# Optimization experiments

Measured on AMD Instinct MI355X. Metric: run time of the kernel, lower is better.

## Reference

```python
import jax, jax.numpy as jnp
import numpy as np

KMEANS_ITERS = 3   # soft-kmeans refinement iterations
TOPK = 12          # hardcoded in the torch module
EPS = 1e-8


def _gather(x, idx):
    # batched_index_select: x (b, c, m); idx (b, n, k) -> (b, c, n, k)
    return jax.vmap(lambda xb, ib: xb[:, ib])(x, idx)


def _soft_kmeans(points, cent):
    # points (b, n, c); cent (b, m, c) -> refined centroids and soft assignment weights (b, n, m)
    for _ in range(KMEANS_ITERS):
        p2 = jnp.sum(points * points, axis=-1)           # (b, n)
        c2 = jnp.sum(cent * cent, axis=-1)               # (b, m)
        logits = -(p2[:, :, None] - 2.0 * jnp.einsum('bnc,bmc->bnm', points, cent) + c2[:, None, :])
        w = jax.nn.softmax(logits, axis=-1)              # (b, n, m)
        cent = jnp.einsum('bnm,bnc->bmc', w, points) / (jnp.sum(w, axis=1)[:, :, None] + EPS)
    return cent, w


def setup_inputs():
    key = jax.random.key(0)
    k1, k2, k3 = jax.random.split(key, 3)
    b, c, H, W, k = 4, 192, 80, 80, 9
    n = H * W
    out_c = 192
    x = jax.random.normal(k1, (b, c, n, 1), dtype=jnp.float32)
    edge_index = jax.random.randint(k2, (2, b, n, k), 0, n)
    conv_w = jax.random.normal(k3, (out_c, 3 * c), dtype=jnp.float32) * (1.0 / np.sqrt(3 * c))
    conv_b = jnp.zeros((out_c,), dtype=jnp.float32)
    return {"x": x, "edge_index": edge_index, "conv_w": conv_w, "conv_b": conv_b,
            "num_centroids": 50, "H": 80, "W": 80}


def reference(x, edge_index, conv_w, conv_b, num_centroids, H, W):
    b, c, n, _ = x.shape
    xs = x[..., 0]                                        # (b, c, n)
    # initial centroids: adaptive_avg_pool2d to (5, 10); H, W chosen divisible so bins are uniform
    x_img = xs.reshape(b, c, H, W)
    init_cent = x_img.reshape(b, c, 5, H // 5, 10, W // 10).mean(axis=(3, 5)).reshape(b, c, 50)
    # edge gathers + max-relative reduction
    x_i = _gather(xs, edge_index[1])                      # (b, c, n, k)
    x_j = _gather(xs, edge_index[0])                      # (b, c, n, k)
    x_j = jnp.max(x_j - x_i, axis=-1, keepdims=True)      # (b, c, n, 1)
    # soft-kmeans centroid construction
    points = jnp.transpose(xs, (0, 2, 1))                 # (b, n, c)
    cent, weights = _soft_kmeans(points, jnp.transpose(init_cent, (0, 2, 1)))
    cent = jnp.transpose(cent, (0, 2, 1))                 # (b, c, m)
    # topk centroid routing + second gather-max stage
    _, nn_idx = jax.lax.top_k(weights, TOPK)              # (b, n, 12)
    x_jc = _gather(cent, nn_idx)                          # (b, c, n, 12)
    x_jc = jnp.max(x_jc - xs[..., None], axis=-1, keepdims=True)  # (b, c, n, 1)
    # channel-interleaved concat (matches torch stack on dim=2 then reshape to 3c)
    feat = jnp.stack([x, x_j, x_jc], axis=2).reshape(b, 3 * c, n)  # (b, 3c, n)
    # BasicConv: 1x1 conv + bias + relu (norm=None)
    out = jnp.einsum('oi,bin->bon', conv_w, feat) + conv_b[None, :, None]
    return jax.nn.relu(out)[..., None]                    # (b, out_c, n, 1)
```

## Files before the change

### kernel.cpp

```cpp
#include <hip/hip_runtime.h>
#include <hip/hip_bf16.h>
#include <math.h>

#define B_   4
#define C_   192
#define N_   6400
#define K_   9
#define M_   50
#define TK_  12
#define OC_  192
#define KC_  576
#define CH_  100
#define LSTR 53
#define TSTR 72
#define XSTR 40
#define GSTR 40
#define FSTR 392

typedef __bf16 b16x8 __attribute__((ext_vector_type(8)));
typedef float f32x4 __attribute__((ext_vector_type(4)));

__device__ inline unsigned short f2b(float f) {
    union { __hip_bfloat16 h; unsigned short u; } v;
    v.h = __float2bfloat16(f);
    return v.u;
}
__device__ inline float b2f(unsigned short u) {
    union { float f; unsigned int i; } v;
    v.i = ((unsigned int)u) << 16;
    return v.f;
}
__device__ inline void up8(uint4 v, float* f) {
    unsigned int w[4] = {v.x, v.y, v.z, v.w};
#pragma unroll
    for (int i = 0; i < 4; i++) {
        f[2 * i]     = b2f((unsigned short)(w[i] & 0xffffu));
        f[2 * i + 1] = b2f((unsigned short)(w[i] >> 16));
    }
}
__device__ inline uint4 pack8(const float* f) {
    unsigned int w[4];
#pragma unroll
    for (int i = 0; i < 4; i++)
        w[i] = (unsigned int)f2b(f[2 * i]) | ((unsigned int)f2b(f[2 * i + 1]) << 16);
    uint4 v; v.x = w[0]; v.y = w[1]; v.z = w[2]; v.w = w[3];
    return v;
}

__global__ void k_transpose(const float* __restrict__ x, float* __restrict__ xt,
                            unsigned short* __restrict__ xt16,
                            unsigned short* __restrict__ xt16l,
                            const float* __restrict__ cw,
                            unsigned short* __restrict__ Wg16) {
    int tid = threadIdx.y * 32 + threadIdx.x;
    if (blockIdx.x >= 200) {
        int g = ((blockIdx.x - 200) * 24 + blockIdx.z * 6 + blockIdx.y) * 256 + tid;
        if (g < OC_ * KC_) {
            int r = g % KC_;
            Wg16[g] = f2b(cw[(g / KC_) * KC_ + (r % C_) * 3 + (r / C_)]);
        }
        return;
    }
    __shared__ float tile[32][33];
    int b = blockIdx.z;
    int p0 = blockIdx.x * 32, c0 = blockIdx.y * 32;
    int tx = threadIdx.x, ty = threadIdx.y;
    const float* xb = x + (size_t)b * C_ * N_;
    float* xtb = xt + (size_t)b * N_ * C_;
    unsigned short* xt16b = xt16 + (size_t)b * N_ * C_;
    unsigned short* xt16lb = xt16l + (size_t)b * N_ * C_;
#pragma unroll
    for (int i = 0; i < 4; i++) {
        int cc = ty + 8 * i;
        tile[cc][tx] = xb[(size_t)(c0 + cc) * N_ + p0 + tx];
    }
    __syncthreads();
#pragma unroll
    for (int i = 0; i < 4; i++) {
        int pp = ty + 8 * i;
        float v = tile[tx][pp];
        size_t o = (size_t)(p0 + pp) * C_ + c0 + tx;
        xtb[o] = v;
        unsigned short hi = f2b(v);
        xt16b[o] = hi;
        xt16lb[o] = f2b(v - b2f(hi));
    }
}

__global__ __launch_bounds__(192) void k_init_cent(const float* __restrict__ xt,
        float* __restrict__ cent, float* __restrict__ c2,
        unsigned short* __restrict__ centh, unsigned short* __restrict__ centl) {
    int m = blockIdx.x, b = blockIdx.y, c = threadIdx.x;
    if (m >= M_) {
        size_t o = ((size_t)b * 64 + m) * C_ + c;
        centh[o] = 0; centl[o] = 0;
        return;
    }
    int gy = m / 10, gx = m % 10;
    const float* xtb = xt + (size_t)b * N_ * C_;
    float s = 0.f;
    for (int yy = 0; yy < 16; yy++)
        for (int xx = 0; xx < 8; xx++) {
            int p = (gy * 16 + yy) * 80 + gx * 8 + xx;
            s += xtb[(size_t)p * C_ + c];
        }
    float v = s * (1.f / 128.f);
    cent[((size_t)b * M_ + m) * C_ + c] = v;
    size_t oh = ((size_t)b * 64 + m) * C_ + c;
    unsigned short hi = f2b(v);
    centh[oh] = hi;
    centl[oh] = f2b(v - b2f(hi));
    float q = v * v;
    __shared__ float red[3];
#pragma unroll
    for (int off = 32; off > 0; off >>= 1) q += __shfl_down(q, off, 64);
    if ((c & 63) == 0) red[c >> 6] = q;
    __syncthreads();
    if (c == 0) c2[(size_t)b * M_ + m] = red[0] + red[1] + red[2];
}

__global__ __launch_bounds__(512) void k_logits_upd(const float* __restrict__ xt,
        const unsigned short* __restrict__ xt16, const unsigned short* __restrict__ xt16l,
        const float* __restrict__ cent,
        const unsigned short* __restrict__ centh, const unsigned short* __restrict__ centl,
        const float* __restrict__ c2g,
        unsigned short* __restrict__ part, float* __restrict__ wsp,
        int* __restrict__ nn, int do_topk, int fast) {
    __shared__ alignas(16) char smem[51712];
    __shared__ float sred[512];
    float* lg = (float*)(smem + 20480);
    unsigned short* lgTh = (unsigned short*)smem;
    unsigned short* lgTl = (unsigned short*)(smem + 9216);
    unsigned short* xTh = (unsigned short*)(smem + 18432);
    unsigned short* xTl = (unsigned short*)(smem + 35072);
    int b = blockIdx.y;
    int blk = blockIdx.x;
    int p0 = blk * 64;
    int tid = threadIdx.x;
    int wave = tid >> 6, lane = tid & 63;
    int m16 = lane & 15, q = lane >> 4;
    const float* xb = xt + ((size_t)b * N_ + p0) * C_;
    const unsigned short* x16b = xt16 + ((size_t)b * N_ + p0) * C_;
    const unsigned short* x16lb = xt16l + ((size_t)b * N_ + p0) * C_;
    if (fast) {
        const unsigned short* chg = centh + (size_t)b * 64 * C_;
        const unsigned short* clg = centl + (size_t)b * 64 * C_;
        int pg = wave & 3, mh = wave >> 2;
        f32x4 acc1[2];
#pragma unroll
        for (int i = 0; i < 2; i++) acc1[i] = (f32x4){0.f, 0.f, 0.f, 0.f};
#pragma unroll
        for (int kt = 0; kt < 6; kt++) {
            int kg = kt * 32;
            size_t xo = (size_t)(pg * 16 + m16) * C_ + kg + q * 8;
            b16x8 bh = *(const b16x8*)&x16b[xo];
            b16x8 bl = *(const b16x8*)&x16lb[xo];
#pragma unroll
            for (int t = 0; t < 2; t++) {
                int mt = mh * 2 + t;
                size_t co = (size_t)(mt * 16 + m16) * C_ + kg + q * 8;
                b16x8 ah = *(const b16x8*)&chg[co];
                b16x8 al = *(const b16x8*)&clg[co];
                acc1[t] = __builtin_amdgcn_mfma_f32_16x16x32_bf16(ah, bh, acc1[t], 0, 0, 0);
                acc1[t] = __builtin_amdgcn_mfma_f32_16x16x32_bf16(ah, bl, acc1[t], 0, 0, 0);
                acc1[t] = __builtin_amdgcn_mfma_f32_16x16x32_bf16(al, bh, acc1[t], 0, 0, 0);
            }
        }
#pragma unroll
        for (int t = 0; t < 2; t++) {
#pragma unroll
            for (int r = 0; r < 4; r++) {
                int m = (mh * 2 + t) * 16 + q * 4 + r;
                if (m < M_) {
                    float c2v = c2g[(size_t)b * M_ + m];
                    lg[(pg * 16 + m16) * LSTR + m] = 2.f * acc1[t][r] - c2v;
                }
            }
        }
    } else {
        const float* cb = cent + (size_t)b * M_ * C_;
        int grp = tid >> 8;
        int ltid = tid & 255;
        int ltx = ltid & 15, lty = ltid >> 4;
        int llr = ltid >> 2, llq = ltid & 3;
        float* Acg = (float*)(smem + grp * 8704);
        float* Bpg = (float*)(smem + grp * 8704 + 4352);
        float acc[4][4];
#pragma unroll
        for (int i = 0; i < 4; i++)
#pragma unroll
            for (int j = 0; j < 4; j++) acc[i][j] = 0.f;
        for (int kt = 0; kt < 6; kt++) {
            int kg = (grp * 6 + kt) * 16;
            float4 cv = make_float4(0.f, 0.f, 0.f, 0.f);
            if (llr < M_) cv = *(const float4*)&cb[(size_t)llr * C_ + kg + 4 * llq];
            float4 pv = *(const float4*)&xb[(size_t)llr * C_ + kg + 4 * llq];
            __syncthreads();
            Acg[(4 * llq + 0) * 68 + llr] = cv.x; Acg[(4 * llq + 1) * 68 + llr] = cv.y;
            Acg[(4 * llq + 2) * 68 + llr] = cv.z; Acg[(4 * llq + 3) * 68 + llr] = cv.w;
            Bpg[(4 * llq + 0) * 68 + llr] = pv.x; Bpg[(4 * llq + 1) * 68 + llr] = pv.y;
            Bpg[(4 * llq + 2) * 68 + llr] = pv.z; Bpg[(4 * llq + 3) * 68 + llr] = pv.w;
            __syncthreads();
#pragma unroll
            for (int kk = 0; kk < 16; kk++) {
                float4 a = *(const float4*)&Acg[kk * 68 + 4 * lty];
                float4 bb = *(const float4*)&Bpg[kk * 68 + 4 * ltx];
                acc[0][0] += a.x * bb.x; acc[0][1] += a.x * bb.y; acc[0][2] += a.x * bb.z; acc[0][3] += a.x * bb.w;
                acc[1][0] += a.y * bb.x; acc[1][1] += a.y * bb.y; acc[1][2] += a.y * bb.z; acc[1][3] += a.y * bb.w;
                acc[2][0] += a.z * bb.x; acc[2][1] += a.z * bb.y; acc[2][2] += a.z * bb.z; acc[2][3] += a.z * bb.w;
                acc[3][0] += a.w * bb.x; acc[3][1] += a.w * bb.y; acc[3][2] += a.w * bb.z; acc[3][3] += a.w * bb.w;
            }
        }
        float* scr = (float*)(smem + 35072);
        if (grp == 1) {
#pragma unroll
            for (int i = 0; i < 4; i++)
#pragma unroll
                for (int j = 0; j < 4; j++) scr[ltid * 16 + i * 4 + j] = acc[i][j];
        }
        __syncthreads();
        if (grp == 0) {
#pragma unroll
            for (int i = 0; i < 4; i++) {
                int m = 4 * lty + i;
                if (m < M_) {
                    float c2v = c2g[(size_t)b * M_ + m];
#pragma unroll
                    for (int j = 0; j < 4; j++) {
                        float t = acc[i][j] + scr[ltid * 16 + i * 4 + j];
                        lg[(4 * ltx + j) * LSTR + m] = 2.f * t - c2v;
                    }
                }
            }
        }
    }
    __syncthreads();
    {
        int p = tid & 63, prt = tid >> 6;
        int m0 = prt * 7;
        int m1 = (m0 + 7 > M_) ? M_ : m0 + 7;
        float* row = &lg[p * LSTR];
        float mx = -1e30f;
        for (int m = m0; m < m1; m++) mx = fmaxf(mx, row[m]);
        sred[prt * 64 + p] = mx;
        __syncthreads();
        mx = -1e30f;
#pragma unroll
        for (int k = 0; k < 8; k++) mx = fmaxf(mx, sred[k * 64 + p]);
        float s = 0.f;
        for (int m = m0; m < m1; m++) {
            float e = expf(row[m] - mx);
            row[m] = e;
            s += e;
        }
        __syncthreads();
        sred[prt * 64 + p] = s;
        __syncthreads();
        s = 0.f;
#pragma unroll
        for (int k = 0; k < 8; k++) s += sred[k * 64 + p];
        float inv = 1.f / s;
        for (int m = m0; m < m1; m++) row[m] *= inv;
    }
    __syncthreads();
    for (int j = tid; j < 64 * 64; j += 512) {
        int m = j >> 6, p = j & 63;
        float w = (m < M_) ? lg[p * LSTR + m] : 0.f;
        unsigned short hi = f2b(w);
        lgTh[m * TSTR + p] = hi;
        lgTl[m * TSTR + p] = f2b(w - b2f(hi));
    }
    __syncthreads();
    if (do_topk && tid < 64) {
        float* row = &lg[tid * LSTR];
        int* nb = nn + ((size_t)b * N_ + p0 + tid) * TK_;
        for (int r = 0; r < TK_; r++) {
            float bv = -1.f;
            int bi = 0;
            for (int m = 0; m < M_; m++) {
                float v = row[m];
                if (v > bv) { bv = v; bi = m; }
            }
            nb[r] = bi;
            row[bi] = -1.f;
        }
    }
    int mt2 = wave >> 1, cbase = (wave & 1) * 7;
    f32x4 acc2[7];
#pragma unroll
    for (int i = 0; i < 7; i++) acc2[i] = (f32x4){0.f, 0.f, 0.f, 0.f};
    for (int h = 0; h < 2; h++) {
        __syncthreads();
        for (int j = tid; j < 32 * 24; j += 512) {
            int pl = j & 31, ko = (j >> 5) * 8;
            int4 vh = *(const int4*)&x16b[(size_t)(h * 32 + pl) * C_ + ko];
            int4 vl = *(const int4*)&x16lb[(size_t)(h * 32 + pl) * C_ + ko];
            const unsigned short* ph = (const unsigned short*)&vh;
            const unsigned short* pv = (const unsigned short*)&vl;
#pragma unroll
            for (int i = 0; i < 8; i++) {
                xTh[(ko + i) * XSTR + pl] = ph[i];
                xTl[(ko + i) * XSTR + pl] = pv[i];
            }
        }
        for (int j = tid; j < 32 * 16; j += 512) {
            int pl = j & 31, c = C_ + (j >> 5);
            xTh[c * XSTR + pl] = (c == C_) ? f2b(1.f) : 0;
            xTl[c * XSTR + pl] = 0;
        }
        __syncthreads();
        b16x8 ah = *(const b16x8*)&lgTh[(mt2 * 16 + m16) * TSTR + h * 32 + q * 8];
        b16x8 al = *(const b16x8*)&lgTl[(mt2 * 16 + m16) * TSTR + h * 32 + q * 8];
#pragma unroll
        for (int ci = 0; ci < 7; ci++) {
            int ct = cbase + ci;
            if (ct >= 13) continue;
            b16x8 bh = *(const b16x8*)&xTh[(ct * 16 + m16) * XSTR + q * 8];
            b16x8 bl = *(const b16x8*)&xTl[(ct * 16 + m16) * XSTR + q * 8];
            acc2[ci] = __builtin_amdgcn_mfma_f32_16x16x32_bf16(ah, bh, acc2[ci], 0, 0, 0);
            acc2[ci] = __builtin_amdgcn_mfma_f32_16x16x32_bf16(ah, bl, acc2[ci], 0, 0, 0);
            acc2[ci] = __builtin_amdgcn_mfma_f32_16x16x32_bf16(al, bh, acc2[ci], 0, 0, 0);
        }
    }
    unsigned short* pb = part + ((size_t)b * CH_ + blk) * (size_t)(M_ * C_);
    int mbase = mt2 * 16 + q * 4;
#pragma unroll
    for (int ci = 0; ci < 7; ci++) {
        int ct = cbase + ci;
        if (ct >= 13) continue;
        int c = ct * 16 + m16;
#pragma unroll
        for (int r = 0; r < 4; r++) {
            int mm = mbase + r;
            if (mm >= M_) continue;
            float v = acc2[ci][r];
            if (c < C_) pb[(size_t)mm * C_ + c] = f2b(v);
            else if (c == C_) wsp[((size_t)b * CH_ + blk) * M_ + mm] = v;
        }
    }
}

__global__ __launch_bounds__(768) void k_upd_reduce(const unsigned short* __restrict__ part,
        const float* __restrict__ wsp, float* __restrict__ cent, float* __restrict__ c2,
        unsigned short* __restrict__ cent16,
        unsigned short* __restrict__ centh, unsigned short* __restrict__ centl, int last) {
    int m = blockIdx.x, b = blockIdx.y;
    int tid = threadIdx.x;
    int c = tid % 192, g = tid / 192;
    __shared__ float pred[3][192];
    __shared__ float sws;
    __shared__ float red[3];
    const unsigned short* pp = part + (((size_t)b * CH_ + (size_t)g * 25) * M_ + m) * (size_t)C_ + c;
    float s = 0.f;
    for (int ch = 0; ch < 25; ch++)
        s += b2f(pp[(size_t)ch * M_ * C_]);
    if (g) pred[g - 1][c] = s;
    if (tid < 64) {
        float w = wsp[((size_t)b * CH_ + tid) * M_ + m];
        if (tid + 64 < CH_) w += wsp[((size_t)b * CH_ + tid + 64) * M_ + m];
#pragma unroll
        for (int off = 32; off > 0; off >>= 1) w += __shfl_down(w, off, 64);
        if (tid == 0) sws = w + 1e-8f;
    }
    __syncthreads();
    if (g == 0) {
        float v = (s + pred[0][c] + pred[1][c] + pred[2][c]) / sws;
        size_t o = ((size_t)b * M_ + m) * C_ + c;
        cent[o] = v;
        if (last) cent16[o] = f2b(v);
        size_t oh = ((size_t)b * 64 + m) * C_ + c;
        unsigned short hi = f2b(v);
        centh[oh] = hi;
        centl[oh] = f2b(v - b2f(hi));
        float q = v * v;
#pragma unroll
        for (int off = 32; off > 0; off >>= 1) q += __shfl_down(q, off, 64);
        if ((c & 63) == 0) red[c >> 6] = q;
    }
    __syncthreads();
    if (tid == 0) c2[(size_t)b * M_ + m] = red[0] + red[1] + red[2];
}

__global__ __launch_bounds__(256) void k_gemm(const unsigned short* __restrict__ Wg16,
        const unsigned short* __restrict__ xt16, const unsigned short* __restrict__ cent16,
        const int* __restrict__ edge, const int* __restrict__ nn,
        const float* __restrict__ bias, float* __restrict__ out) {
    __shared__ alignas(16) char smem[65536];
    unsigned short* feat = (unsigned short*)smem;
    int* sidx = (int*)(smem + 50176);
    short* As = (short*)(smem + 50176);
    int bid = blockIdx.x;
    int xcd = bid & 7;
    int b = xcd >> 1;
    int po = ((xcd & 1) * 50 + (bid >> 3)) * 64;
    int tid = threadIdx.x;
    int wave = tid >> 6, lane = tid & 63;
    int m16 = lane & 15, q = lane >> 4;
    const unsigned short* xb = xt16 + (size_t)b * N_ * C_;
    const unsigned short* cb = cent16 + (size_t)b * M_ * C_;
    for (int j = tid; j < 64 * 30; j += 256) {
        int g = j / 30, r = j % 30;
        size_t base = (size_t)b * N_ + po + g;
        int v;
        if (r < K_) v = edge[base * K_ + r];
        else if (r < 2 * K_) v = edge[(size_t)B_ * N_ * K_ + base * K_ + (r - K_)];
        else v = nn[base * TK_ + (r - 2 * K_)];
        sidx[j] = v;
    }
    __syncthreads();
#pragma unroll
    for (int r6 = 0; r6 < 6; r6++) {
        int j = r6 * 256 + tid;
        int g = j / 24, t = j % 24;
        int ch0 = t * 8;
        const int* si = &sidx[g * 30];
        int p = po + g;
        float xv[8], ta[8], tb[8], mj[8], mc[8];
        up8(*(const uint4*)&xb[(size_t)p * C_ + ch0], xv);
#pragma unroll
        for (int e = 0; e < 8; e++) { mj[e] = -1e30f; mc[e] = -1e30f; }
#pragma unroll
        for (int kk = 0; kk < K_; kk++) {
            up8(*(const uint4*)&xb[(size_t)si[kk] * C_ + ch0], ta);
            up8(*(const uint4*)&xb[(size_t)si[K_ + kk] * C_ + ch0], tb);
#pragma unroll
            for (int e = 0; e < 8; e++) mj[e] = fmaxf(mj[e], ta[e] - tb[e]);
        }
#pragma unroll
        for (int kk = 0; kk < TK_; kk++) {
            up8(*(const uint4*)&cb[(size_t)si[2 * K_ + kk] * C_ + ch0], ta);
#pragma unroll
            for (int e = 0; e < 8; e++) mc[e] = fmaxf(mc[e], ta[e]);
        }
#pragma unroll
        for (int e = 0; e < 8; e++) mc[e] -= xv[e];
        *(uint4*)&feat[(size_t)g * FSTR + ch0] = pack8(mj);
        *(uint4*)&feat[(size_t)g * FSTR + 192 + ch0] = pack8(mc);
    }
    f32x4 acc[12];
#pragma unroll
    for (int i = 0; i < 12; i++) acc[i] = (f32x4){0.f, 0.f, 0.f, 0.f};
    for (int kt = 0; kt < 18; kt++) {
        int kg = kt * 32;
        int4 av[3];
#pragma unroll
        for (int t = 0; t < 3; t++) {
            int idx = t * 256 + tid;
            av[t] = *(const int4*)&Wg16[(size_t)(idx >> 2) * KC_ + kg + (idx & 3) * 8];
        }
        __syncthreads();
#pragma unroll
        for (int t = 0; t < 3; t++) {
            int idx = t * 256 + tid;
            *(int4*)&As[(idx >> 2) * GSTR + (idx & 3) * 8] = av[t];
        }
        __syncthreads();
        b16x8 bf;
        if (kt < 6)
            bf = *(const b16x8*)&xb[(size_t)(po + wave * 16 + m16) * C_ + kg + q * 8];
        else
            bf = *(const b16x8*)&feat[(size_t)(wave * 16 + m16) * FSTR + (kg - C_) + q * 8];
#pragma unroll
        for (int of = 0; of < 12; of++) {
            b16x8 af = *(const b16x8*)&As[(of * 16 + m16) * GSTR + q * 8];
            acc[of] = __builtin_amdgcn_mfma_f32_16x16x32_bf16(af, bf, acc[of], 0, 0, 0);
        }
    }
    int p = po + wave * 16 + m16;
#pragma unroll
    for (int of = 0; of < 12; of++) {
        int o = of * 16 + q * 4;
        float4 bv = *(const float4*)&bias[o];
        float bia[4] = {bv.x, bv.y, bv.z, bv.w};
#pragma unroll
        for (int r = 0; r < 4; r++)
            out[((size_t)b * OC_ + o + r) * N_ + p] = fmaxf(acc[of][r] + bia[r], 0.f);
    }
}

extern "C" void kernel_launch(void* const* d_in, const int* in_sizes, int n_in,
                              void* d_out, int out_size, void* d_ws, size_t ws_size,
                              hipStream_t stream) {
    (void)in_sizes; (void)n_in; (void)out_size; (void)ws_size;
    const float* x   = (const float*)d_in[0];
    const int* edge  = (const int*)d_in[1];
    const float* cw  = (const float*)d_in[2];
    const float* cbi = (const float*)d_in[3];
    float* ws = (float*)d_ws;
    size_t o = 0;
    float* xt   = ws + o; o += (size_t)B_ * N_ * C_;
    unsigned short* xt16 = (unsigned short*)(ws + o); o += (size_t)B_ * N_ * C_ / 2;
    unsigned short* xt16l = (unsigned short*)(ws + o); o += (size_t)B_ * N_ * C_ / 2;
    unsigned short* Wg16 = (unsigned short*)(ws + o); o += (size_t)OC_ * KC_ / 2;
    float* cent = ws + o; o += (size_t)B_ * M_ * C_;
    unsigned short* cent16 = (unsigned short*)(ws + o); o += (size_t)B_ * M_ * C_ / 2;
    unsigned short* centh = (unsigned short*)(ws + o); o += (size_t)B_ * 64 * C_ / 2;
    unsigned short* centl = (unsigned short*)(ws + o); o += (size_t)B_ * 64 * C_ / 2;
    float* c2   = ws + o; o += (size_t)B_ * M_;
    unsigned short* part = (unsigned short*)(ws + o); o += (size_t)B_ * CH_ * M_ * C_ / 2;
    float* wsp  = ws + o; o += (size_t)B_ * CH_ * M_;
    int* nn = (int*)(ws + o); o += (size_t)B_ * N_ * TK_;
    float* outp = (float*)d_out;

    k_transpose<<<dim3(218, C_ / 32, B_), dim3(32, 8), 0, stream>>>(x, xt, xt16, xt16l, cw, Wg16);
    k_init_cent<<<dim3(64, B_), dim3(192), 0, stream>>>(xt, cent, c2, centh, centl);
    for (int it = 0; it < 3; it++) {
        k_logits_upd<<<dim3(CH_, B_), dim3(512), 0, stream>>>(xt, xt16, xt16l, cent,
            centh, centl, c2, part, wsp, nn, (it == 2) ? 1 : 0, (it < 2) ? 1 : 0);
        k_upd_reduce<<<dim3(M_, B_), dim3(768), 0, stream>>>(part, wsp, cent, c2,
            cent16, centh, centl, (it == 2) ? 1 : 0);
    }
    k_gemm<<<dim3(400), dim3(256), 0, stream>>>(Wg16, xt16, cent16, edge, nn, cbi, outp);
}
```

Measured before the change: 250.4 us.

## Prefetch weights in 96-wide K chunks and hoist B fragments into registers

Restructures the GEMM stage of k_gemm. It stages 96 columns of the weight matrix per step instead of 32, which cuts the barrier pairs from 18 to 5. The next chunk is prefetched into registers while MFMAs run on the current one, and the first chunk's load is issued before the gather phase. The x and feat B-fragments are loaded into registers up front, so the A tile can reuse the feat shared memory region, which shrinks the LDS allocation. The cost is higher VGPR pressure (9 int4 prefetch registers plus 18 b16x8 fragments), which may lower occupancy.

```diff
diff --git a/kernel.cpp b/kernel.cpp
--- a/kernel.cpp
+++ b/kernel.cpp
@@ -14,7 +14,7 @@
 #define LSTR 53
 #define TSTR 72
 #define XSTR 40
-#define GSTR 40
+#define ASTR 104
 #define FSTR 392
 
 typedef __bf16 b16x8 __attribute__((ext_vector_type(8)));
@@ -385,10 +385,10 @@
         const unsigned short* __restrict__ xt16, const unsigned short* __restrict__ cent16,
         const int* __restrict__ edge, const int* __restrict__ nn,
         const float* __restrict__ bias, float* __restrict__ out) {
-    __shared__ alignas(16) char smem[65536];
+    __shared__ alignas(16) char smem[57856];
     unsigned short* feat = (unsigned short*)smem;
+    short* As = (short*)smem;
     int* sidx = (int*)(smem + 50176);
-    short* As = (short*)(smem + 50176);
     int bid = blockIdx.x;
     int xcd = bid & 7;
     int b = xcd >> 1;
@@ -398,6 +398,19 @@
     int m16 = lane & 15, q = lane >> 4;
     const unsigned short* xb = xt16 + (size_t)b * N_ * C_;
     const unsigned short* cb = cent16 + (size_t)b * M_ * C_;
+    int4 av[9];
+#pragma unroll
+    for (int t = 0; t < 9; t++) {
+        int idx = t * 256 + tid;
+        av[t] = *(const int4*)&Wg16[(size_t)(idx / 12) * KC_ + (idx % 12) * 8];
+    }
+    b16x8 bx0, bx1, bx2, bx3, bx4, bx5;
+    {
+        const unsigned short* xr = &xb[(size_t)(po + wave * 16 + m16) * C_ + q * 8];
+        bx0 = *(const b16x8*)&xr[0];   bx1 = *(const b16x8*)&xr[32];
+        bx2 = *(const b16x8*)&xr[64];  bx3 = *(const b16x8*)&xr[96];
+        bx4 = *(const b16x8*)&xr[128]; bx5 = *(const b16x8*)&xr[160];
+    }
     for (int j = tid; j < 64 * 30; j += 256) {
         int g = j / 30, r = j % 30;
         size_t base = (size_t)b * N_ + po + g;
@@ -437,33 +450,52 @@
         *(uint4*)&feat[(size_t)g * FSTR + ch0] = pack8(mj);
         *(uint4*)&feat[(size_t)g * FSTR + 192 + ch0] = pack8(mc);
     }
+    __syncthreads();
+    b16x8 bfr[12];
+    {
+        const unsigned short* fr = &feat[(size_t)(wave * 16 + m16) * FSTR + q * 8];
+#pragma unroll
+        for (int f = 0; f < 12; f++)
+            bfr[f] = *(const b16x8*)&fr[f * 32];
+    }
+    __syncthreads();
+#pragma unroll
+    for (int t = 0; t < 9; t++) {
+        int idx = t * 256 + tid;
+        *(int4*)&As[(idx / 12) * ASTR + (idx % 12) * 8] = av[t];
+    }
+    __syncthreads();
     f32x4 acc[12];
 #pragma unroll
     for (int i = 0; i < 12; i++) acc[i] = (f32x4){0.f, 0.f, 0.f, 0.f};
-    for (int kt = 0; kt < 18; kt++) {
-        int kg = kt * 32;
-        int4 av[3];
-#pragma unroll
-        for (int t = 0; t < 3; t++) {
-            int idx = t * 256 + tid;
-            av[t] = *(const int4*)&Wg16[(size_t)(idx >> 2) * KC_ + kg + (idx & 3) * 8];
-        }
-        __syncthreads();
-#pragma unroll
-        for (int t = 0; t < 3; t++) {
-            int idx = t * 256 + tid;
-            *(int4*)&As[(idx >> 2) * GSTR + (idx & 3) * 8] = av[t];
-        }
-        __syncthreads();
-        b16x8 bf;
-        if (kt < 6)
-            bf = *(const b16x8*)&xb[(size_t)(po + wave * 16 + m16) * C_ + kg + q * 8];
-        else
-            bf = *(const b16x8*)&feat[(size_t)(wave * 16 + m16) * FSTR + (kg - C_) + q * 8];
-#pragma unroll
-        for (int of = 0; of < 12; of++) {
-            b16x8 af = *(const b16x8*)&As[(of * 16 + m16) * GSTR + q * 8];
-            acc[of] = __builtin_amdgcn_mfma_f32_16x16x32_bf16(af, bf, acc[of], 0, 0, 0);
+#pragma unroll
+    for (int c = 0; c < 6; c++) {
+        if (c < 5) {
+#pragma unroll
+            for (int t = 0; t < 9; t++) {
+                int idx = t * 256 + tid;
+                av[t] = *(const int4*)&Wg16[(size_t)(idx / 12) * KC_ + (c + 1) * 96 + (idx % 12) * 8];
+            }
+        }
+#pragma unroll
+        for (int ks = 0; ks < 3; ks++) {
+            int f = c * 3 + ks;
+            b16x8 bf = (f == 0) ? bx0 : (f == 1) ? bx1 : (f == 2) ? bx2 :
+                       (f == 3) ? bx3 : (f == 4) ? bx4 : (f == 5) ? bx5 : bfr[f - 6];
+#pragma unroll
+            for (int of = 0; of < 12; of++) {
+                b16x8 af = *(const b16x8*)&As[(of * 16 + m16) * ASTR + ks * 32 + q * 8];
+                acc[of] = __builtin_amdgcn_mfma_f32_16x16x32_bf16(af, bf, acc[of], 0, 0, 0);
+            }
+        }
+        if (c < 5) {
+            __syncthreads();
+#pragma unroll
+            for (int t = 0; t < 9; t++) {
+                int idx = t * 256 + tid;
+                *(int4*)&As[(idx / 12) * ASTR + (idx % 12) * 8] = av[t];
+            }
+            __syncthreads();
         }
     }
     int p = po + wave * 16 + m16;
```

Result: no change. 247.7 us (-1.1%).
